# Kernel optimization log

Measured on AMD Instinct MI355X. Metric: run time of the kernel, lower is better.

The kernel has to match this reference:

```python
import jax, jax.numpy as jnp
import numpy as np

STATE_DIM = 128
EDGE_DIM = 32
INNER_DIM = 256
B, N = 32, 128


def _lin_params(key, fan_in, fan_out):
    kw, kb = jax.random.split(key)
    bound = 1.0 / np.sqrt(fan_in)
    W = jax.random.uniform(kw, (fan_in, fan_out), minval=-bound, maxval=bound, dtype=jnp.float32)
    b = jax.random.uniform(kb, (fan_out,), minval=-bound, maxval=bound, dtype=jnp.float32)
    return W, b


def setup_inputs() -> dict:
    key = jax.random.key(0)
    ks = jax.random.split(key, 10)
    h = jax.random.normal(ks[0], (B, N, STATE_DIM), dtype=jnp.float32)
    edge_feat = jax.random.normal(ks[1], (B, N, N, EDGE_DIM), dtype=jnp.float32)
    edge_mask = jax.random.uniform(ks[2], (B, N, N), dtype=jnp.float32)
    in_dim = 2 * STATE_DIM + EDGE_DIM
    Wm1, bm1 = _lin_params(ks[3], in_dim, INNER_DIM)
    Wm2, bm2 = _lin_params(ks[4], INNER_DIM, STATE_DIM)
    Wg1, bg1 = _lin_params(ks[5], in_dim, INNER_DIM)
    Wg2, bg2 = _lin_params(ks[6], INNER_DIM, 1)
    Wu1, bu1 = _lin_params(ks[7], 2 * STATE_DIM + 1, INNER_DIM)
    Wu2, bu2 = _lin_params(ks[8], INNER_DIM, STATE_DIM)
    ln_w = jnp.ones((STATE_DIM,), jnp.float32)
    ln_b = jnp.zeros((STATE_DIM,), jnp.float32)
    return dict(h=h, edge_feat=edge_feat, edge_mask=edge_mask,
                Wm1=Wm1, bm1=bm1, Wm2=Wm2, bm2=bm2,
                Wg1=Wg1, bg1=bg1, Wg2=Wg2, bg2=bg2,
                Wu1=Wu1, bu1=bu1, Wu2=Wu2, bu2=bu2,
                ln_w=ln_w, ln_b=ln_b)


def _layernorm(x, w, b, eps=1e-5):
    mu = jnp.mean(x, axis=-1, keepdims=True)
    var = jnp.mean((x - mu) ** 2, axis=-1, keepdims=True)
    return (x - mu) * jax.lax.rsqrt(var + eps) * w + b


def reference(h, edge_feat, edge_mask,
              Wm1, bm1, Wm2, bm2,
              Wg1, bg1, Wg2, bg2,
              Wu1, bu1, Wu2, bu2,
              ln_w, ln_b):
    n = h.shape[1]
    # all-pairs concat [B,N,N,2*state+edge]; h_i broadcast over axis 2, h_j over axis 1
    h_i = jnp.broadcast_to(h[:, :, None, :], (h.shape[0], n, n, h.shape[-1]))
    h_j = jnp.broadcast_to(h[:, None, :, :], (h.shape[0], n, n, h.shape[-1]))
    pair = jnp.concatenate([h_i, h_j, edge_feat], axis=-1)
    gate = jax.nn.sigmoid(jnp.tanh(pair @ Wg1 + bg1) @ Wg2 + bg2) * edge_mask[..., None]
    msg = jnp.tanh(pair @ Wm1 + bm1) @ Wm2 + bm2
    denom = jnp.maximum(jnp.sum(gate, axis=2), 1.0)  # [B,N,1]
    agg = jnp.sum(gate * msg, axis=2) / denom  # [B,N,state]
    degree = jnp.sum(edge_mask, axis=-1, keepdims=True)
    degree_norm = degree / max(n - 1, 1)
    upd_in = jnp.concatenate([h, agg, degree_norm], axis=-1)
    delta = jnp.tanh(jnp.tanh(upd_in @ Wu1 + bu1) @ Wu2 + bu2)
    return _layernorm(h + delta, ln_w, ln_b)
```

## Files before the change

kernel.cpp:

```cpp
#include <hip/hip_runtime.h>
#include <hip/hip_bf16.h>

#define BB 32
#define NN 128
#define SD 128
#define ED 32
#define ID 256
#define BN (BB*NN)
#define NI 4

#define WM2B 288
#define WU1B 352
#define WU2B 480

typedef __attribute__((ext_vector_type(8))) short sh8;
typedef __attribute__((ext_vector_type(4))) float f32x4;

__device__ __forceinline__ float ftanh(float x) {
    float e2 = __expf(2.0f * x);
    return 1.0f - 2.0f * __builtin_amdgcn_rcpf(e2 + 1.0f);
}

__device__ __forceinline__ ushort f2bf(float f) {
    unsigned u = __float_as_uint(f);
    return (ushort)((u + 0x7FFF + ((u >> 16) & 1)) >> 16);
}

__device__ __forceinline__ sh8 afragT(const float* base, int stride, int kt, int lane) {
    sh8 v = (sh8){0, 0, 0, 0, 0, 0, 0, 0};
    if ((lane & 15) < 4) {
        const float* p = base + (lane & 15) * stride + kt * 32 + (lane >> 4) * 8;
        f32x4 a0 = *(const f32x4*)p;
        f32x4 a1 = *(const f32x4*)(p + 4);
        v[0] = (short)f2bf(a0[0]); v[1] = (short)f2bf(a0[1]);
        v[2] = (short)f2bf(a0[2]); v[3] = (short)f2bf(a0[3]);
        v[4] = (short)f2bf(a1[0]); v[5] = (short)f2bf(a1[1]);
        v[6] = (short)f2bf(a1[2]); v[7] = (short)f2bf(a1[3]);
    }
    return v;
}

__global__ void k_prep(const float* __restrict__ Wg1, const float* __restrict__ Wm1,
                       const float* __restrict__ Wm2, const float* __restrict__ Wu1,
                       const float* __restrict__ Wu2, ushort* __restrict__ Bprep) {
    const int tt = blockIdx.x;
    const int l = threadIdx.x;
    const float* W;
    int rowbase, nt, stride;
    if (tt < 256) {
        const int tgt = tt >> 6;
        const int kt = (tt >> 4) & 3;
        nt = tt & 15;
        W = (tgt >= 2) ? Wm1 : Wg1;
        rowbase = (tgt & 1) * 128 + kt * 32;
        stride = ID;
    } else if (tt < WM2B) {
        const int wt = tt - 256;
        W = (wt >> 4) ? Wm1 : Wg1;
        rowbase = 2 * SD;
        nt = wt & 15;
        stride = ID;
    } else if (tt < WU1B) {
        const int wt = tt - WM2B;
        W = Wm2; rowbase = (wt >> 3) * 32; nt = wt & 7; stride = SD;
    } else if (tt < WU2B) {
        const int wt = tt - WU1B;
        W = Wu1; rowbase = (wt >> 4) * 32; nt = wt & 15; stride = ID;
    } else {
        const int wt = tt - WU2B;
        W = Wu2; rowbase = (wt >> 3) * 32; nt = wt & 7; stride = SD;
    }
    const int colw = nt * 16 + (l & 15);
    const int kb = rowbase + (l >> 4) * 8;
    sh8 v;
    #pragma unroll
    for (int e = 0; e < 8; ++e)
        v[e] = (short)f2bf(W[(size_t)(kb + e) * stride + colw]);
    *(sh8*)&Bprep[(size_t)tt * 512 + l * 8] = v;
}

__global__ __launch_bounds__(256) void k1_mfma(
        const float* __restrict__ h,
        const float* __restrict__ bg1, const float* __restrict__ bm1,
        const ushort* __restrict__ Bprep,
        float* __restrict__ Hgi, float* __restrict__ Hgjt,
        float* __restrict__ Hmi, float* __restrict__ Hmjt) {
    const int blk = blockIdx.x;
    const int tgt = blockIdx.y;
    const int t = threadIdx.x;
    const int w = t >> 6;
    const int lane = t & 63;
    const int col = lane & 15;
    const int grp = lane >> 4;
    __shared__ __align__(16) ushort Alds[4 * 512];

    {
        const int c = t;
        const int kt = c >> 6, l = c & 63;
        const int row = l & 15;
        const int kb = kt * 32 + (l >> 4) * 8;
        const float* p = h + (size_t)(blk * 16 + row) * SD + kb;
        f32x4 a0 = *(const f32x4*)p;
        f32x4 a1 = *(const f32x4*)(p + 4);
        sh8 v;
        v[0] = (short)f2bf(a0[0]); v[1] = (short)f2bf(a0[1]);
        v[2] = (short)f2bf(a0[2]); v[3] = (short)f2bf(a0[3]);
        v[4] = (short)f2bf(a1[0]); v[5] = (short)f2bf(a1[1]);
        v[6] = (short)f2bf(a1[2]); v[7] = (short)f2bf(a1[3]);
        *(sh8*)&Alds[c * 8] = v;
    }
    __syncthreads();

    const int kcol = w * 64 + col;
    sh8 Af[4];
    #pragma unroll
    for (int kt = 0; kt < 4; ++kt)
        Af[kt] = *(const sh8*)&Alds[kt * 512 + lane * 8];

    f32x4 acc[4];
    #pragma unroll
    for (int n = 0; n < 4; ++n) acc[n] = (f32x4){0.f, 0.f, 0.f, 0.f};
    #pragma unroll
    for (int kt = 0; kt < 4; ++kt)
        #pragma unroll
        for (int n = 0; n < 4; ++n) {
            sh8 Bf = *(const sh8*)&Bprep[
                (size_t)(tgt * 64 + kt * 16 + w * 4 + n) * 512 + lane * 8];
            acc[n] = __builtin_amdgcn_mfma_f32_16x16x32_bf16(
                Af[kt], Bf, acc[n], 0, 0, 0);
        }
    if (tgt & 1) {
        float* out = (tgt == 1) ? Hgjt : Hmjt;
        #pragma unroll
        for (int n = 0; n < 4; ++n)
            *(f32x4*)&out[((size_t)blk * ID + kcol + n * 16) * 16 + grp * 4] = acc[n];
    } else {
        const float* bias = (tgt == 0) ? bg1 : bm1;
        float* out = (tgt == 0) ? Hgi : Hmi;
        #pragma unroll
        for (int n = 0; n < 4; ++n) {
            const float bv = bias[kcol + n * 16];
            #pragma unroll
            for (int r = 0; r < 4; ++r)
                out[(size_t)(blk * 16 + grp * 4 + r) * ID + kcol + n * 16] =
                    acc[n][r] + bv;
        }
    }
}

__global__ __launch_bounds__(256, 4) void k2_fused(
        const float* __restrict__ ef, const float* __restrict__ em,
        const ushort* __restrict__ Bprep,
        const float* __restrict__ Hgi, const float* __restrict__ Hmi,
        const float* __restrict__ Hgjt, const float* __restrict__ Hmjt,
        const float* __restrict__ Wg2, const float* __restrict__ bg2,
        const float* __restrict__ h,
        const float* __restrict__ Wu1, const float* __restrict__ bu1,
        const float* __restrict__ bu2, const float* __restrict__ bm2,
        const float* __restrict__ lnw, const float* __restrict__ lnb,
        float* __restrict__ out) {
    const int bi0 = blockIdx.x * NI;
    const int b = bi0 >> 7;
    const int t = threadIdx.x;
    const int w = t >> 6;
    const int lane = t & 63;
    const int col = lane & 15;
    const int grp = lane >> 4;

    __shared__ __align__(16) ushort Elds[NI * 8 * 512];
    __shared__ float glds[NI][NN];
    __shared__ float red[2][4][2];
    __shared__ float gsumL[NI], degL[NI];

    {
        float* gl = &glds[0][0];
        gl[t] = 0.f;
        gl[t + 256] = 0.f;
    }
    #pragma unroll
    for (int i = 0; i < NI; ++i) {
        const float* efb = ef + (size_t)(bi0 + i) * NN * ED;
        #pragma unroll
        for (int it = 0; it < 2; ++it) {
            const int c = it * 256 + t;
            const int j = ((c >> 6) << 4) | (c & 15);
            const int kb = ((c >> 4) & 3) * 8;
            const float* p = efb + j * ED + kb;
            f32x4 a0 = *(const f32x4*)p;
            f32x4 a1 = *(const f32x4*)(p + 4);
            sh8 v;
            v[0] = (short)f2bf(a0[0]); v[1] = (short)f2bf(a0[1]);
            v[2] = (short)f2bf(a0[2]); v[3] = (short)f2bf(a0[3]);
            v[4] = (short)f2bf(a1[0]); v[5] = (short)f2bf(a1[1]);
            v[6] = (short)f2bf(a1[2]); v[7] = (short)f2bf(a1[3]);
            *(sh8*)&Elds[i * 4096 + c * 8] = v;
        }
    }
    __syncthreads();

    const int kcol = w * 64 + col;
    sh8 Bg[4], Bm[4];
    #pragma unroll
    for (int n = 0; n < 4; ++n) {
        Bg[n] = *(const sh8*)&Bprep[(size_t)(256 + w * 4 + n) * 512 + lane * 8];
        Bm[n] = *(const sh8*)&Bprep[(size_t)(272 + w * 4 + n) * 512 + lane * 8];
    }
    const float* HgjL = Hgjt + (size_t)b * 8 * ID * 16 + (size_t)kcol * 16 + grp * 4;
    const float* HmjL = Hmjt + (size_t)b * 8 * ID * 16 + (size_t)kcol * 16 + grp * 4;

    {
        float hgiR[NI][4], wg2R[4];
        #pragma unroll
        for (int n = 0; n < 4; ++n) wg2R[n] = Wg2[kcol + n * 16];
        #pragma unroll
        for (int i = 0; i < NI; ++i)
            #pragma unroll
            for (int n = 0; n < 4; ++n)
                hgiR[i][n] = Hgi[(size_t)(bi0 + i) * ID + kcol + n * 16];
        f32x4 Cg[4], Cn[4];
        #pragma unroll
        for (int n = 0; n < 4; ++n) Cg[n] = *(const f32x4*)(HgjL + n * 256);
        for (int s = 0; s < 8; ++s) {
            if (s < 7) {
                const float* ps = HgjL + (s + 1) * (ID * 16);
                #pragma unroll
                for (int n = 0; n < 4; ++n) Cn[n] = *(const f32x4*)(ps + n * 256);
            }
            #pragma unroll
            for (int i = 0; i < NI; ++i) {
                sh8 Af = *(const sh8*)&Elds[i * 4096 + s * 512 + lane * 8];
                f32x4 acc[4];
                #pragma unroll
                for (int n = 0; n < 4; ++n)
                    acc[n] = __builtin_amdgcn_mfma_f32_16x16x32_bf16(
                        Af, Bg[n], Cg[n], 0, 0, 0);
                float p[4] = {0.f, 0.f, 0.f, 0.f};
                #pragma unroll
                for (int n = 0; n < 4; ++n)
                    #pragma unroll
                    for (int r = 0; r < 4; ++r)
                        p[r] = fmaf(ftanh(acc[n][r] + hgiR[i][n]), wg2R[n], p[r]);
                #pragma unroll
                for (int m = 1; m < 16; m <<= 1)
                    #pragma unroll
                    for (int r = 0; r < 4; ++r) p[r] += __shfl_xor(p[r], m, 64);
                if (col == 0) {
                    #pragma unroll
                    for (int r = 0; r < 4; ++r)
                        atomicAdd(&glds[i][s * 16 + grp * 4 + r], p[r]);
                }
            }
            #pragma unroll
            for (int n = 0; n < 4; ++n) Cg[n] = Cn[n];
        }
    }
    __syncthreads();

    {
        const float bg2v = bg2[0];
        #pragma unroll
        for (int it = 0; it < NI / 2; ++it) {
            const int i = it * 2 + (t >> 7);
            const int j = t & 127;
            const float pre = glds[i][j] + bg2v;
            const float m = em[(size_t)(bi0 + i) * NN + j];
            const float g = m * __builtin_amdgcn_rcpf(1.0f + __expf(-pre));
            glds[i][j] = g;
            float gsv = g, dv = m;
            #pragma unroll
            for (int mm = 1; mm < 64; mm <<= 1) {
                gsv += __shfl_xor(gsv, mm, 64);
                dv  += __shfl_xor(dv, mm, 64);
            }
            if (lane == 0) { red[it][w][0] = gsv; red[it][w][1] = dv; }
        }
    }
    __syncthreads();
    if (t < NI) {
        const int it = t >> 1, w0 = (t & 1) * 2;
        gsumL[t] = red[it][w0][0] + red[it][w0 + 1][0];
        degL[t]  = red[it][w0][1] + red[it][w0 + 1][1];
    }

    float ts[NI][4];
    {
        float hmiR[NI][4];
        #pragma unroll
        for (int i = 0; i < NI; ++i)
            #pragma unroll
            for (int n = 0; n < 4; ++n)
                hmiR[i][n] = Hmi[(size_t)(bi0 + i) * ID + kcol + n * 16];
        #pragma unroll
        for (int i = 0; i < NI; ++i)
            #pragma unroll
            for (int n = 0; n < 4; ++n) ts[i][n] = 0.f;
        f32x4 Cm[4], Cn[4];
        #pragma unroll
        for (int n = 0; n < 4; ++n) Cm[n] = *(const f32x4*)(HmjL + n * 256);
        for (int s = 0; s < 8; ++s) {
            if (s < 7) {
                const float* ps = HmjL + (s + 1) * (ID * 16);
                #pragma unroll
                for (int n = 0; n < 4; ++n) Cn[n] = *(const f32x4*)(ps + n * 256);
            }
            #pragma unroll
            for (int i = 0; i < NI; ++i) {
                sh8 Af = *(const sh8*)&Elds[i * 4096 + s * 512 + lane * 8];
                f32x4 acc[4];
                #pragma unroll
                for (int n = 0; n < 4; ++n)
                    acc[n] = __builtin_amdgcn_mfma_f32_16x16x32_bf16(
                        Af, Bm[n], Cm[n], 0, 0, 0);
                f32x4 gr = *(const f32x4*)&glds[i][s * 16 + grp * 4];
                #pragma unroll
                for (int n = 0; n < 4; ++n)
                    #pragma unroll
                    for (int r = 0; r < 4; ++r)
                        ts[i][n] = fmaf(gr[r], ftanh(acc[n][r] + hmiR[i][n]),
                                        ts[i][n]);
            }
            #pragma unroll
            for (int n = 0; n < 4; ++n) Cm[n] = Cn[n];
        }
        #pragma unroll
        for (int i = 0; i < NI; ++i)
            #pragma unroll
            for (int n = 0; n < 4; ++n) {
                ts[i][n] += __shfl_xor(ts[i][n], 16, 64);
                ts[i][n] += __shfl_xor(ts[i][n], 32, 64);
            }
    }

    __syncthreads();
    float* scratch = (float*)Elds;
    float* Tl  = scratch;
    float* up  = scratch + 1024;
    float* uu  = scratch + 2064;
    float* xsb = scratch + 3088;
    if (lane < 16) {
        #pragma unroll
        for (int i = 0; i < NI; ++i)
            #pragma unroll
            for (int n = 0; n < 4; ++n)
                Tl[i * 256 + w * 64 + n * 16 + lane] = ts[i][n];
    }
    #pragma unroll
    for (int it = 0; it < 2; ++it) {
        const int idx = it * 256 + t;
        const int i = idx >> 7, c = idx & 127;
        up[i * 260 + c] = h[(size_t)(bi0 + i) * SD + c];
    }
    if (t < NI) up[t * 260 + 256] = degL[t] * (1.0f / 127.0f);
    __syncthreads();

    {
        f32x4 acc[2];
        acc[0] = (f32x4){0.f, 0.f, 0.f, 0.f};
        acc[1] = (f32x4){0.f, 0.f, 0.f, 0.f};
        #pragma unroll
        for (int kt = 0; kt < 8; ++kt) {
            sh8 Af = afragT(Tl, 256, kt, lane);
            #pragma unroll
            for (int n2 = 0; n2 < 2; ++n2) {
                sh8 Bf = *(const sh8*)&Bprep[
                    (size_t)(WM2B + kt * 8 + w * 2 + n2) * 512 + lane * 8];
                acc[n2] = __builtin_amdgcn_mfma_f32_16x16x32_bf16(Af, Bf, acc[n2], 0, 0, 0);
            }
        }
        if (grp == 0) {
            #pragma unroll
            for (int n2 = 0; n2 < 2; ++n2) {
                const int d = (w * 2 + n2) * 16 + lane;
                const float bmv = bm2[d];
                #pragma unroll
                for (int r = 0; r < 4; ++r) {
                    const float g = gsumL[r];
                    up[r * 260 + SD + d] = fmaf(g, bmv, acc[n2][r]) *
                                           __builtin_amdgcn_rcpf(fmaxf(g, 1.0f));
                }
            }
        }
    }
    __syncthreads();

    {
        f32x4 acc[4];
        #pragma unroll
        for (int n2 = 0; n2 < 4; ++n2) acc[n2] = (f32x4){0.f, 0.f, 0.f, 0.f};
        #pragma unroll
        for (int kt = 0; kt < 8; ++kt) {
            sh8 Af = afragT(up, 260, kt, lane);
            #pragma unroll
            for (int n2 = 0; n2 < 4; ++n2) {
                sh8 Bf = *(const sh8*)&Bprep[
                    (size_t)(WU1B + kt * 16 + w * 4 + n2) * 512 + lane * 8];
                acc[n2] = __builtin_amdgcn_mfma_f32_16x16x32_bf16(Af, Bf, acc[n2], 0, 0, 0);
            }
        }
        if (grp == 0) {
            #pragma unroll
            for (int n2 = 0; n2 < 4; ++n2) {
                const int kc = (w * 4 + n2) * 16 + lane;
                const float wdeg = Wu1[(size_t)(2 * SD) * ID + kc];
                const float bb = bu1[kc];
                #pragma unroll
                for (int r = 0; r < 4; ++r)
                    uu[r * 256 + kc] =
                        ftanh(acc[n2][r] + bb + up[r * 260 + 256] * wdeg);
            }
        }
    }
    __syncthreads();

    {
        f32x4 acc[2];
        acc[0] = (f32x4){0.f, 0.f, 0.f, 0.f};
        acc[1] = (f32x4){0.f, 0.f, 0.f, 0.f};
        #pragma unroll
        for (int kt = 0; kt < 8; ++kt) {
            sh8 Af = afragT(uu, 256, kt, lane);
            #pragma unroll
            for (int n2 = 0; n2 < 2; ++n2) {
                sh8 Bf = *(const sh8*)&Bprep[
                    (size_t)(WU2B + kt * 8 + w * 2 + n2) * 512 + lane * 8];
                acc[n2] = __builtin_amdgcn_mfma_f32_16x16x32_bf16(Af, Bf, acc[n2], 0, 0, 0);
            }
        }
        if (grp == 0) {
            #pragma unroll
            for (int n2 = 0; n2 < 2; ++n2) {
                const int d = (w * 2 + n2) * 16 + lane;
                const float bb = bu2[d];
                #pragma unroll
                for (int r = 0; r < 4; ++r)
                    xsb[r * 128 + d] = up[r * 260 + d] + ftanh(acc[n2][r] + bb);
            }
        }
    }
    __syncthreads();

    {
        const float v0 = xsb[w * 128 + lane], v1 = xsb[w * 128 + lane + 64];
        float s = v0 + v1;
        #pragma unroll
        for (int m = 1; m < 64; m <<= 1) s += __shfl_xor(s, m, 64);
        const float mu = s * (1.0f / SD);
        const float d0 = v0 - mu, d1 = v1 - mu;
        float q = d0 * d0 + d1 * d1;
        #pragma unroll
        for (int m = 1; m < 64; m <<= 1) q += __shfl_xor(q, m, 64);
        const float inv = rsqrtf(q * (1.0f / SD) + 1e-5f);
        out[(size_t)(bi0 + w) * SD + lane] = d0 * inv * lnw[lane] + lnb[lane];
        out[(size_t)(bi0 + w) * SD + lane + 64] =
            d1 * inv * lnw[lane + 64] + lnb[lane + 64];
    }
}

extern "C" void kernel_launch(void* const* d_in, const int* in_sizes, int n_in,
                              void* d_out, int out_size, void* d_ws, size_t ws_size,
                              hipStream_t stream) {
    const float* h   = (const float*)d_in[0];
    const float* ef  = (const float*)d_in[1];
    const float* em  = (const float*)d_in[2];
    const float* Wm1 = (const float*)d_in[3];
    const float* bm1 = (const float*)d_in[4];
    const float* Wm2 = (const float*)d_in[5];
    const float* bm2 = (const float*)d_in[6];
    const float* Wg1 = (const float*)d_in[7];
    const float* bg1 = (const float*)d_in[8];
    const float* Wg2 = (const float*)d_in[9];
    const float* bg2 = (const float*)d_in[10];
    const float* Wu1 = (const float*)d_in[11];
    const float* bu1 = (const float*)d_in[12];
    const float* Wu2 = (const float*)d_in[13];
    const float* bu2 = (const float*)d_in[14];
    const float* lnw = (const float*)d_in[15];
    const float* lnb = (const float*)d_in[16];

    float* ws = (float*)d_ws;
    float* Hgi   = ws;
    float* Hgjt  = Hgi + (size_t)BN * ID;
    float* Hmi   = Hgjt + (size_t)BN * ID;
    float* Hmjt  = Hmi + (size_t)BN * ID;
    ushort* Bprep = (ushort*)(Hmjt + (size_t)BN * ID);
    float* outp = (float*)d_out;

    k_prep<<<544, 64, 0, stream>>>(Wg1, Wm1, Wm2, Wu1, Wu2, Bprep);
    k1_mfma<<<dim3(BN / 16, 4), 256, 0, stream>>>(h, bg1, bm1, Bprep,
                                                  Hgi, Hgjt, Hmi, Hmjt);
    k2_fused<<<BN / NI, 256, 0, stream>>>(ef, em, Bprep, Hgi, Hmi, Hgjt, Hmjt,
                                          Wg2, bg2, h, Wu1, bu1, bu2, bm2,
                                          lnw, lnb, outp);
}
```

Before: 120.0 us.

## Split edge-tile processing into two j-halves to halve LDS and raise occupancy

New measurement: 256.8 us. 2.14x slower.

```diff
diff --git a/kernel.cpp b/kernel.cpp
--- a/kernel.cpp
+++ b/kernel.cpp
@@ -148,7 +148,7 @@
     }
 }
 
-__global__ __launch_bounds__(256, 4) void k2_fused(
+__global__ __launch_bounds__(256, 8) void k2_fused(
         const float* __restrict__ ef, const float* __restrict__ em,
         const ushort* __restrict__ Bprep,
         const float* __restrict__ Hgi, const float* __restrict__ Hmi,
@@ -167,9 +167,8 @@
     const int col = lane & 15;
     const int grp = lane >> 4;
 
-    __shared__ __align__(16) ushort Elds[NI * 8 * 512];
+    __shared__ __align__(16) ushort Elds[NI * 4 * 512];
     __shared__ float glds[NI][NN];
-    __shared__ float red[2][4][2];
     __shared__ float gsumL[NI], degL[NI];
 
     {
@@ -177,13 +176,26 @@
         gl[t] = 0.f;
         gl[t + 256] = 0.f;
     }
-    #pragma unroll
-    for (int i = 0; i < NI; ++i) {
-        const float* efb = ef + (size_t)(bi0 + i) * NN * ED;
-        #pragma unroll
-        for (int it = 0; it < 2; ++it) {
-            const int c = it * 256 + t;
-            const int j = ((c >> 6) << 4) | (c & 15);
+
+    const int kcol = w * 64 + col;
+    const float* HgjL = Hgjt + (size_t)b * 8 * ID * 16 + (size_t)kcol * 16 + grp * 4;
+    const float* HmjL = Hmjt + (size_t)b * 8 * ID * 16 + (size_t)kcol * 16 + grp * 4;
+    const float bg2v = bg2[0];
+
+    float ts[NI][4];
+    #pragma unroll
+    for (int i = 0; i < NI; ++i)
+        #pragma unroll
+        for (int n = 0; n < 4; ++n) ts[i][n] = 0.f;
+    float gs_run = 0.f, dv_run = 0.f;
+
+    for (int half = 0; half < 2; ++half) {
+        __syncthreads();
+        #pragma unroll
+        for (int i = 0; i < NI; ++i) {
+            const float* efb = ef + (size_t)(bi0 + i) * NN * ED;
+            const int c = t;
+            const int j = (half * 4 + (c >> 6)) * 16 + (c & 15);
             const int kb = ((c >> 4) & 3) * 8;
             const float* p = efb + j * ED + kb;
             f32x4 a0 = *(const f32x4*)p;
@@ -193,143 +205,132 @@
             v[2] = (short)f2bf(a0[2]); v[3] = (short)f2bf(a0[3]);
             v[4] = (short)f2bf(a1[0]); v[5] = (short)f2bf(a1[1]);
             v[6] = (short)f2bf(a1[2]); v[7] = (short)f2bf(a1[3]);
-            *(sh8*)&Elds[i * 4096 + c * 8] = v;
-        }
-    }
-    __syncthreads();
-
-    const int kcol = w * 64 + col;
-    sh8 Bg[4], Bm[4];
-    #pragma unroll
-    for (int n = 0; n < 4; ++n) {
-        Bg[n] = *(const sh8*)&Bprep[(size_t)(256 + w * 4 + n) * 512 + lane * 8];
-        Bm[n] = *(const sh8*)&Bprep[(size_t)(272 + w * 4 + n) * 512 + lane * 8];
-    }
-    const float* HgjL = Hgjt + (size_t)b * 8 * ID * 16 + (size_t)kcol * 16 + grp * 4;
-    const float* HmjL = Hmjt + (size_t)b * 8 * ID * 16 + (size_t)kcol * 16 + grp * 4;
-
-    {
-        float hgiR[NI][4], wg2R[4];
-        #pragma unroll
-        for (int n = 0; n < 4; ++n) wg2R[n] = Wg2[kcol + n * 16];
-        #pragma unroll
-        for (int i = 0; i < NI; ++i)
+            *(sh8*)&Elds[i * 2048 + c * 8] = v;
+        }
+        __syncthreads();
+
+        {
+            sh8 Bg[4];
+            float hgiR[NI][4], wg2R[4];
+            #pragma unroll
+            for (int n = 0; n < 4; ++n) {
+                Bg[n] = *(const sh8*)&Bprep[(size_t)(256 + w * 4 + n) * 512 + lane * 8];
+                wg2R[n] = Wg2[kcol + n * 16];
+            }
+            #pragma unroll
+            for (int i = 0; i < NI; ++i)
+                #pragma unroll
+                for (int n = 0; n < 4; ++n)
+                    hgiR[i][n] = Hgi[(size_t)(bi0 + i) * ID + kcol + n * 16];
+            const float* Hbase = HgjL + (size_t)(half * 4) * (ID * 16);
+            f32x4 Cg[4], Cn[4];
+            #pragma unroll
+            for (int n = 0; n < 4; ++n) Cg[n] = *(const f32x4*)(Hbase + n * 256);
+            for (int st = 0; st < 4; ++st) {
+                if (st < 3) {
+                    const float* ps = Hbase + (size_t)(st + 1) * (ID * 16);
+                    #pragma unroll
+                    for (int n = 0; n < 4; ++n) Cn[n] = *(const f32x4*)(ps + n * 256);
+                }
+                #pragma unroll
+                for (int i = 0; i < NI; ++i) {
+                    sh8 Af = *(const sh8*)&Elds[i * 2048 + st * 512 + lane * 8];
+                    f32x4 acc[4];
+                    #pragma unroll
+                    for (int n = 0; n < 4; ++n)
+                        acc[n] = __builtin_amdgcn_mfma_f32_16x16x32_bf16(
+                            Af, Bg[n], Cg[n], 0, 0, 0);
+                    float p[4] = {0.f, 0.f, 0.f, 0.f};
+                    #pragma unroll
+                    for (int n = 0; n < 4; ++n)
+                        #pragma unroll
+                        for (int r = 0; r < 4; ++r)
+                            p[r] = fmaf(ftanh(acc[n][r] + hgiR[i][n]), wg2R[n], p[r]);
+                    #pragma unroll
+                    for (int m = 1; m < 16; m <<= 1)
+                        #pragma unroll
+                        for (int r = 0; r < 4; ++r) p[r] += __shfl_xor(p[r], m, 64);
+                    if (col == 0) {
+                        #pragma unroll
+                        for (int r = 0; r < 4; ++r)
+                            atomicAdd(&glds[i][(half * 4 + st) * 16 + grp * 4 + r],
+                                      p[r]);
+                    }
+                }
+                #pragma unroll
+                for (int n = 0; n < 4; ++n) Cg[n] = Cn[n];
+            }
+        }
+        __syncthreads();
+
+        {
+            const int j = half * 64 + lane;
+            const float pre = glds[w][j] + bg2v;
+            const float m = em[(size_t)(bi0 + w) * NN + j];
+            const float g = m * __builtin_amdgcn_rcpf(1.0f + __expf(-pre));
+            glds[w][j] = g;
+            gs_run += g;
+            dv_run += m;
+        }
+        __syncthreads();
+
+        {
+            sh8 Bm[4];
+            float hmiR[NI][4];
             #pragma unroll
             for (int n = 0; n < 4; ++n)
-                hgiR[i][n] = Hgi[(size_t)(bi0 + i) * ID + kcol + n * 16];
-        f32x4 Cg[4], Cn[4];
-        #pragma unroll
-        for (int n = 0; n < 4; ++n) Cg[n] = *(const f32x4*)(HgjL + n * 256);
-        for (int s = 0; s < 8; ++s) {
-            if (s < 7) {
-                const float* ps = HgjL + (s + 1) * (ID * 16);
-                #pragma unroll
-                for (int n = 0; n < 4; ++n) Cn[n] = *(const f32x4*)(ps + n * 256);
-            }
-            #pragma unroll
-            for (int i = 0; i < NI; ++i) {
-                sh8 Af = *(const sh8*)&Elds[i * 4096 + s * 512 + lane * 8];
-                f32x4 acc[4];
+                Bm[n] = *(const sh8*)&Bprep[(size_t)(272 + w * 4 + n) * 512 + lane * 8];
+            #pragma unroll
+            for (int i = 0; i < NI; ++i)
                 #pragma unroll
                 for (int n = 0; n < 4; ++n)
-                    acc[n] = __builtin_amdgcn_mfma_f32_16x16x32_bf16(
-                        Af, Bg[n], Cg[n], 0, 0, 0);
-                float p[4] = {0.f, 0.f, 0.f, 0.f};
-                #pragma unroll
-                for (int n = 0; n < 4; ++n)
-                    #pragma unroll
-                    for (int r = 0; r < 4; ++r)
-                        p[r] = fmaf(ftanh(acc[n][r] + hgiR[i][n]), wg2R[n], p[r]);
-                #pragma unroll
-                for (int m = 1; m < 16; m <<= 1)
-                    #pragma unroll
-                    for (int r = 0; r < 4; ++r) p[r] += __shfl_xor(p[r], m, 64);
-                if (col == 0) {
-                    #pragma unroll
-                    for (int r = 0; r < 4; ++r)
-                        atomicAdd(&glds[i][s * 16 + grp * 4 + r], p[r]);
+                    hmiR[i][n] = Hmi[(size_t)(bi0 + i) * ID + kcol + n * 16];
+            const float* Hbase = HmjL + (size_t)(half * 4) * (ID * 16);
+            f32x4 Cm[4], Cn[4];
+            #pragma unroll
+            for (int n = 0; n < 4; ++n) Cm[n] = *(const f32x4*)(Hbase + n * 256);
+            for (int st = 0; st < 4; ++st) {
+                if (st < 3) {
+                    const float* ps = Hbase + (size_t)(st + 1) * (ID * 16);
+                    #pragma unroll
+                    for (int n = 0; n < 4; ++n) Cn[n] = *(const f32x4*)(ps + n * 256);
                 }
-            }
-            #pragma unroll
-            for (int n = 0; n < 4; ++n) Cg[n] = Cn[n];
-        }
-    }
-    __syncthreads();
-
-    {
-        const float bg2v = bg2[0];
-        #pragma unroll
-        for (int it = 0; it < NI / 2; ++it) {
-            const int i = it * 2 + (t >> 7);
-            const int j = t & 127;
-            const float pre = glds[i][j] + bg2v;
-            const float m = em[(size_t)(bi0 + i) * NN + j];
-            const float g = m * __builtin_amdgcn_rcpf(1.0f + __expf(-pre));
-            glds[i][j] = g;
-            float gsv = g, dv = m;
-            #pragma unroll
-            for (int mm = 1; mm < 64; mm <<= 1) {
-                gsv += __shfl_xor(gsv, mm, 64);
-                dv  += __shfl_xor(dv, mm, 64);
-            }
-            if (lane == 0) { red[it][w][0] = gsv; red[it][w][1] = dv; }
-        }
-    }
-    __syncthreads();
-    if (t < NI) {
-        const int it = t >> 1, w0 = (t & 1) * 2;
-        gsumL[t] = red[it][w0][0] + red[it][w0 + 1][0];
-        degL[t]  = red[it][w0][1] + red[it][w0 + 1][1];
-    }
-
-    float ts[NI][4];
-    {
-        float hmiR[NI][4];
-        #pragma unroll
-        for (int i = 0; i < NI; ++i)
-            #pragma unroll
-            for (int n = 0; n < 4; ++n)
-                hmiR[i][n] = Hmi[(size_t)(bi0 + i) * ID + kcol + n * 16];
-        #pragma unroll
-        for (int i = 0; i < NI; ++i)
-            #pragma unroll
-            for (int n = 0; n < 4; ++n) ts[i][n] = 0.f;
-        f32x4 Cm[4], Cn[4];
-        #pragma unroll
-        for (int n = 0; n < 4; ++n) Cm[n] = *(const f32x4*)(HmjL + n * 256);
-        for (int s = 0; s < 8; ++s) {
-            if (s < 7) {
-                const float* ps = HmjL + (s + 1) * (ID * 16);
-                #pragma unroll
-                for (int n = 0; n < 4; ++n) Cn[n] = *(const f32x4*)(ps + n * 256);
-            }
-            #pragma unroll
-            for (int i = 0; i < NI; ++i) {
-                sh8 Af = *(const sh8*)&Elds[i * 4096 + s * 512 + lane * 8];
-                f32x4 acc[4];
-                #pragma unroll
-                for (int n = 0; n < 4; ++n)
-                    acc[n] = __builtin_amdgcn_mfma_f32_16x16x32_bf16(
-                        Af, Bm[n], Cm[n], 0, 0, 0);
-                f32x4 gr = *(const f32x4*)&glds[i][s * 16 + grp * 4];
-                #pragma unroll
-                for (int n = 0; n < 4; ++n)
-                    #pragma unroll
-                    for (int r = 0; r < 4; ++r)
-                        ts[i][n] = fmaf(gr[r], ftanh(acc[n][r] + hmiR[i][n]),
-                                        ts[i][n]);
-            }
-            #pragma unroll
-            for (int n = 0; n < 4; ++n) Cm[n] = Cn[n];
-        }
-        #pragma unroll
-        for (int i = 0; i < NI; ++i)
-            #pragma unroll
-            for (int n = 0; n < 4; ++n) {
-                ts[i][n] += __shfl_xor(ts[i][n], 16, 64);
-                ts[i][n] += __shfl_xor(ts[i][n], 32, 64);
-            }
-    }
+                #pragma unroll
+                for (int i = 0; i < NI; ++i) {
+                    sh8 Af = *(const sh8*)&Elds[i * 2048 + st * 512 + lane * 8];
+                    f32x4 acc[4];
+                    #pragma unroll
+                    for (int n = 0; n < 4; ++n)
+                        acc[n] = __builtin_amdgcn_mfma_f32_16x16x32_bf16(
+                            Af, Bm[n], Cm[n], 0, 0, 0);
+                    f32x4 gr = *(const f32x4*)&glds[i][(half * 4 + st) * 16 + grp * 4];
+                    #pragma unroll
+                    for (int n = 0; n < 4; ++n)
+                        #pragma unroll
+                        for (int r = 0; r < 4; ++r)
+                            ts[i][n] = fmaf(gr[r], ftanh(acc[n][r] + hmiR[i][n]),
+                                            ts[i][n]);
+                }
+                #pragma unroll
+                for (int n = 0; n < 4; ++n) Cm[n] = Cn[n];
+            }
+        }
+    }
+
+    #pragma unroll
+    for (int mm = 1; mm < 64; mm <<= 1) {
+        gs_run += __shfl_xor(gs_run, mm, 64);
+        dv_run += __shfl_xor(dv_run, mm, 64);
+    }
+    if (lane == 0) { gsumL[w] = gs_run; degL[w] = dv_run; }
+
+    #pragma unroll
+    for (int i = 0; i < NI; ++i)
+        #pragma unroll
+        for (int n = 0; n < 4; ++n) {
+            ts[i][n] += __shfl_xor(ts[i][n], 16, 64);
+            ts[i][n] += __shfl_xor(ts[i][n], 32, 64);
+        }
 
     __syncthreads();
     float* scratch = (float*)Elds;
```
